# Performance work log

Hardware: AMD Instinct MI355X
Metric: run time of the kernel (lower is better)

The kernel has to match this reference:

```python
import jax, jax.numpy as jnp
import numpy as np

B, T, IN, HID, OUT, NB = 64, 150, 120, 1024, 35, 8
VTH = 1.0


def _branch_mask(rng, out_dim, in_size):
    # For each output neuron: a random permutation of inputs split into NB equal branches.
    perm = np.argsort(rng.random((out_dim, in_size)), axis=1)          # [out, in]
    branch = (np.arange(in_size) * NB) // in_size                      # branch id of each slot
    rows = (np.arange(out_dim)[:, None] * NB + branch[None, :]).ravel()
    m = np.zeros((out_dim * NB, in_size), dtype=np.bool_)
    m[rows, perm.ravel()] = True
    return jnp.asarray(m)


def setup_inputs() -> dict:
    rng = np.random.default_rng(0)

    def lin(o, i):
        bound = 1.0 / np.sqrt(i)
        w = rng.uniform(-bound, bound, (o, i)).astype(np.float32)
        b = rng.uniform(-bound, bound, (o,)).astype(np.float32)
        return jnp.asarray(w), jnp.asarray(b)

    def tau(*shape):
        return jnp.asarray(rng.uniform(0.0, 4.0, shape).astype(np.float32))

    w1, b1 = lin(HID * NB, IN)
    w2, b2 = lin(HID * NB, HID)
    w3, b3 = lin(HID * NB, HID)
    wr, br = lin(OUT, HID)

    x = jax.random.normal(jax.random.key(0), (B, 1, T, IN), dtype=jnp.float32)

    return dict(
        x=x,
        w1=w1, b1=b1, tau_m1=tau(HID), tau_n1=tau(HID, NB),
        w2=w2, b2=b2, tau_m2=tau(HID), tau_n2=tau(HID, NB),
        w3=w3, b3=b3, tau_m3=tau(HID), tau_n3=tau(HID, NB),
        wr=wr, br=br, tau_mr=tau(OUT),
        mask1=_branch_mask(rng, HID, IN),
        mask2=_branch_mask(rng, HID, HID),
        mask3=_branch_mask(rng, HID, HID),
    )


@jax.custom_vjp
def act_fun(x):  # spike with rectangular surrogate gradient
    return (x > 0.0).astype(x.dtype)

def _act_fwd(x):
    return act_fun(x), x

def _act_bwd(x, g):
    return (g * (jnp.abs(x) < 0.5).astype(g.dtype),)

act_fun.defvjp(_act_fwd, _act_bwd)


def _dh_step(spk_in, d, mem, spk, wm, b, tau_m, tau_n):
    # wm: pre-masked weight [HID*NB, D_in]
    dense = (spk_in @ wm.T + b).reshape(-1, HID, NB)      # [B, HID, NB]
    beta = jax.nn.sigmoid(tau_n)                          # [HID, NB]
    d = beta * d + (1.0 - beta) * dense                   # branch decay
    l_input = d.sum(axis=2)                               # [B, HID]
    alpha = jax.nn.sigmoid(tau_m)
    mem = mem * alpha + (1.0 - alpha) * l_input - VTH * spk  # soft reset (prev spike)
    spk = act_fun(mem - VTH)
    return d, mem, spk


def _forward(x, w1, b1, tau_m1, tau_n1, w2, b2, tau_m2, tau_n2,
             w3, b3, tau_m3, tau_n3, wr, br, tau_mr, mask1, mask2, mask3):
    b_sz = x.shape[0]
    wm1 = w1 * mask1.astype(w1.dtype)
    wm2 = w2 * mask2.astype(w2.dtype)
    wm3 = w3 * mask3.astype(w3.dtype)
    alpha_r = jax.nn.sigmoid(tau_mr)

    xt = x[:, 0].transpose(1, 0, 2)                        # [T, B, IN]

    z_bh = jnp.zeros((b_sz, HID), x.dtype)
    z_bhn = jnp.zeros((b_sz, HID, NB), x.dtype)
    carry0 = (z_bhn, z_bh, z_bh, z_bhn, z_bh, z_bh, z_bhn, z_bh, z_bh,
              jnp.zeros((b_sz, OUT), x.dtype), jnp.zeros((b_sz, OUT), x.dtype))

    def step(carry, inp_t):
        d1, m1, s1, d2, m2, s2, d3, m3, s3, mr, acc = carry
        d1, m1, s1 = _dh_step(inp_t, d1, m1, s1, wm1, b1, tau_m1, tau_n1)
        d2, m2, s2 = _dh_step(s1,    d2, m2, s2, wm2, b2, tau_m2, tau_n2)
        d3, m3, s3 = _dh_step(s2,    d3, m3, s3, wm3, b3, tau_m3, tau_n3)
        mr = mr * alpha_r + (1.0 - alpha_r) * (s3 @ wr.T + br)
        acc = acc + mr
        return (d1, m1, s1, d2, m2, s2, d3, m3, s3, mr, acc), None

    (_, _, _, _, _, _, _, _, _, _, acc), _ = jax.lax.scan(step, carry0, xt)
    return jax.nn.log_softmax(acc / xt.shape[0], axis=1)


def reference(x, w1, b1, tau_m1, tau_n1, w2, b2, tau_m2, tau_n2,
              w3, b3, tau_m3, tau_n3, wr, br, tau_mr, mask1, mask2, mask3):
    return _forward(x, w1, b1, tau_m1, tau_n1, w2, b2, tau_m2, tau_n2,
                    w3, b3, tau_m3, tau_n3, wr, br, tau_mr, mask1, mask2, mask3)
```

## Files before the change

### kernel.cpp

```cpp
#include <hip/hip_runtime.h>
#include <stdint.h>

#define BATCH 64
#define TT    150
#define INSZ  120
#define HID   1024
#define OUTN  35
#define NBR   8
#define TPAD  160
#define CH    8
#define NCHUNK 19

typedef __attribute__((address_space(4))) const uint64_t cu64;

#define XT_OFF  0
#define S1_OFF  4608000
#define S2_OFF  5918720
#define S3_OFF  7229440
#define Y_OFF   8540160
#define ACC_OFF 9884160

__global__ __launch_bounds__(256) void k_tx(const float* __restrict__ x,
                                            float* __restrict__ xT) {
    const int t = blockIdx.x;
    __shared__ float tile[INSZ * 65];
    for (int e = threadIdx.x; e < INSZ * 64; e += 256) {
        const int b = e / INSZ, i = e - b * INSZ;
        tile[i * 65 + b] = x[((size_t)b * TT + t) * INSZ + i];
    }
    __syncthreads();
    for (int e = threadIdx.x; e < INSZ * 64; e += 256) {
        const int i = e >> 6, b = e & 63;
        xT[((size_t)t * INSZ + i) * 64 + b] = tile[i * 65 + b];
    }
}

template <int DIN, int NNZ, int MODE>
__global__ __launch_bounds__(512, 8) void k_layer(
    const float* __restrict__ w,
    const void* __restrict__ maskp,
    const float* __restrict__ bias,
    const float* __restrict__ tau_m,
    const float* __restrict__ tau_n,
    const float* __restrict__ xin,
    const uint64_t* __restrict__ inm,
    uint64_t* __restrict__ outm)
{
    const int tid  = threadIdx.x;
    const int lane = tid & 63;
    const int wid  = tid >> 6;
    const int h    = blockIdx.x;
    const int r    = h * NBR + wid;

    __shared__ uint2 ent[NBR * NNZ];
    __shared__ float red[2][NBR * CH * 64];

    inm = (const uint64_t*)__builtin_assume_aligned(inm, 64);

    const unsigned char* m8  = (const unsigned char*)maskp;
    const int*           m32 = (const int*)maskp;
    {
        const int base = wid * NNZ;
        int cnt = 0;
        for (int c = 0; c * 64 < DIN; ++c) {
            const int i = c * 64 + lane;
            int   mv = 0;
            float wv = 0.f;
            if (i < DIN) {
                mv = m8[(size_t)r * DIN + i];
                wv = w[(size_t)r * DIN + i];
            }
            const unsigned long long bal = __ballot(mv != 0);
            const int pos = __popcll(bal & ((1ull << lane) - 1ull));
            if (mv && cnt + pos < NNZ)
                ent[base + cnt + pos] = make_uint2(__float_as_uint(wv), (unsigned)i);
            cnt += __popcll(bal);
        }
        if (cnt != NNZ) {
            cnt = 0;
            for (int c = 0; c * 64 < DIN; ++c) {
                const int i = c * 64 + lane;
                int   mv = 0;
                float wv = 0.f;
                if (i < DIN) {
                    mv = m32[(size_t)r * DIN + i];
                    wv = w[(size_t)r * DIN + i];
                }
                const unsigned long long bal = __ballot(mv != 0);
                const int pos = __popcll(bal & ((1ull << lane) - 1ull));
                if (mv) ent[base + cnt + pos] =
                            make_uint2(__float_as_uint(wv), (unsigned)i);
                cnt += __popcll(bal);
            }
        }
    }
    __syncthreads();

    const float be = 1.f / (1.f + expf(-tau_n[r]));
    const float om = 1.f - be;
    const float bb = bias[r];
    const float al  = 1.f / (1.f + expf(-tau_m[h]));
    const float oma = 1.f - al;

    float d = 0.f, mem = 0.f, spkprev = 0.f;
    const int base = wid * NNZ;

    for (int tc = 0; tc < NCHUNK; ++tc) {
        const int t0  = tc * CH;
        const int buf = tc & 1;
        float a[CH];
#pragma unroll
        for (int k = 0; k < CH; ++k) a[k] = 0.f;

        if constexpr (MODE == 1) {
#pragma unroll 4
            for (int j = 0; j < NNZ; ++j) {
                const uint2 e  = ent[base + j];
                const int   ix = __builtin_amdgcn_readfirstlane((int)e.y);
                const float wv = __uint_as_float(e.x);
                const cu64* p = (const cu64*)(inm + (size_t)ix * TPAD + t0);
                uint64_t m[CH];
#pragma unroll
                for (int k = 0; k < CH; ++k) m[k] = p[k];
#pragma unroll
                for (int k = 0; k < CH; ++k) {
                    float s;
                    asm("v_cndmask_b32 %0, 0, %1, %2"
                        : "=v"(s) : "v"(wv), "s"(m[k]));
                    a[k] += s;
                }
            }
        } else {
            const float* xb = xin + (size_t)t0 * DIN * 64;
#pragma unroll 3
            for (int j = 0; j < NNZ; ++j) {
                const uint2 e  = ent[base + j];
                const int   ix = __builtin_amdgcn_readfirstlane((int)e.y);
                const float wv = __uint_as_float(e.x);
#pragma unroll
                for (int k = 0; k < CH; ++k)
                    a[k] += wv * xb[((size_t)k * DIN + ix) * 64 + lane];
            }
        }

#pragma unroll
        for (int k = 0; k < CH; ++k) {
            d = be * d + om * (a[k] + bb);
            red[buf][(wid * CH + k) * 64 + lane] = d;
        }
        __syncthreads();

        if (wid == 0) {
#pragma unroll
            for (int k = 0; k < CH; ++k) {
                const float r0 = red[buf][(0 * CH + k) * 64 + lane];
                const float r1 = red[buf][(1 * CH + k) * 64 + lane];
                const float r2 = red[buf][(2 * CH + k) * 64 + lane];
                const float r3 = red[buf][(3 * CH + k) * 64 + lane];
                const float r4 = red[buf][(4 * CH + k) * 64 + lane];
                const float r5 = red[buf][(5 * CH + k) * 64 + lane];
                const float r6 = red[buf][(6 * CH + k) * 64 + lane];
                const float r7 = red[buf][(7 * CH + k) * 64 + lane];
                const float p01 = r0 + r1, p23 = r2 + r3;
                const float p45 = r4 + r5, p67 = r6 + r7;
                const float l = ((p01 + p23) + p45) + p67;
                if (t0 + k < TT) {
                    mem = al * mem + oma * l - spkprev;
                    spkprev = (mem > 1.0f) ? 1.f : 0.f;
                    const unsigned long long bal = __ballot(mem > 1.0f);
                    if (lane == 0) outm[(size_t)h * TPAD + (t0 + k)] = bal;
                }
            }
        }
    }
}

__global__ __launch_bounds__(256) void k_ry(const float* __restrict__ wr,
                                            const uint64_t* __restrict__ s3m,
                                            float* __restrict__ Y) {
    const int lane  = threadIdx.x & 63;
    const int wid   = __builtin_amdgcn_readfirstlane(threadIdx.x >> 6);
    const int o  = blockIdx.x / NCHUNK;
    const int t0 = (blockIdx.x % NCHUNK) * CH;
    s3m = (const uint64_t*)__builtin_assume_aligned(s3m, 64);
    const float* wrow = wr + (size_t)o * HID;
    __shared__ float red[4 * CH * 64];
    float acc[CH];
#pragma unroll
    for (int k = 0; k < CH; ++k) acc[k] = 0.f;
#pragma unroll 4
    for (int ii = 0; ii < HID / 4; ++ii) {
        const int i = wid * (HID / 4) + ii;
        const float wv = wrow[i];
        const cu64* p = (const cu64*)(s3m + (size_t)i * TPAD + t0);
        uint64_t m[CH];
#pragma unroll
        for (int k = 0; k < CH; ++k) m[k] = p[k];
#pragma unroll
        for (int k = 0; k < CH; ++k) {
            float s;
            asm("v_cndmask_b32 %0, 0, %1, %2" : "=v"(s) : "v"(wv), "s"(m[k]));
            acc[k] += s;
        }
    }
#pragma unroll
    for (int k = 0; k < CH; ++k)
        red[(wid * CH + k) * 64 + lane] = acc[k];
    __syncthreads();
    if (wid == 0) {
#pragma unroll
        for (int k = 0; k < CH; ++k) {
            if (t0 + k >= TT) break;
            const float v = ((red[(0 * CH + k) * 64 + lane]
                            + red[(1 * CH + k) * 64 + lane])
                            + red[(2 * CH + k) * 64 + lane])
                            + red[(3 * CH + k) * 64 + lane];
            Y[((size_t)(t0 + k) * OUTN + o) * 64 + lane] = v;
        }
    }
}

__global__ void k_racc(const float* __restrict__ Y,
                       const float* __restrict__ br,
                       const float* __restrict__ tau_mr,
                       float* __restrict__ ACC) {
    const int o = blockIdx.x, lane = threadIdx.x;
    const float ar  = 1.f / (1.f + expf(-tau_mr[o]));
    const float bro = br[o];
    float acc = 0.f, q = ar;
    for (int t = TT - 1; t >= 0; --t) {
        const float y = Y[((size_t)t * OUTN + o) * 64 + lane] + bro;
        acc += y * (1.f - q);
        q *= ar;
    }
    ACC[o * 64 + lane] = acc;
}

__global__ void k_smax(const float* __restrict__ ACC, float* __restrict__ out) {
    const int b = threadIdx.x;
    float v[OUTN];
    float mx = -3.4e38f;
    for (int o = 0; o < OUTN; ++o) {
        v[o] = ACC[o * 64 + b] / (float)TT;
        mx = fmaxf(mx, v[o]);
    }
    float sum = 0.f;
    for (int o = 0; o < OUTN; ++o) sum += expf(v[o] - mx);
    const float lse = mx + logf(sum);
    for (int o = 0; o < OUTN; ++o) out[b * OUTN + o] = v[o] - lse;
}

extern "C" void kernel_launch(void* const* d_in, const int* in_sizes, int n_in,
                              void* d_out, int out_size, void* d_ws,
                              size_t ws_size, hipStream_t stream) {
    (void)in_sizes; (void)n_in; (void)out_size; (void)ws_size;
    const float* x   = (const float*)d_in[0];
    const float* w1  = (const float*)d_in[1];
    const float* b1  = (const float*)d_in[2];
    const float* tm1 = (const float*)d_in[3];
    const float* tn1 = (const float*)d_in[4];
    const float* w2  = (const float*)d_in[5];
    const float* b2  = (const float*)d_in[6];
    const float* tm2 = (const float*)d_in[7];
    const float* tn2 = (const float*)d_in[8];
    const float* w3  = (const float*)d_in[9];
    const float* b3  = (const float*)d_in[10];
    const float* tm3 = (const float*)d_in[11];
    const float* tn3 = (const float*)d_in[12];
    const float* wr  = (const float*)d_in[13];
    const float* br  = (const float*)d_in[14];
    const float* tmr = (const float*)d_in[15];
    const void*  m1  = d_in[16];
    const void*  m2  = d_in[17];
    const void*  m3  = d_in[18];
    float* out = (float*)d_out;

    char* ws = (char*)d_ws;
    float*    xT  = (float*)(ws + XT_OFF);
    uint64_t* s1m = (uint64_t*)(ws + S1_OFF);
    uint64_t* s2m = (uint64_t*)(ws + S2_OFF);
    uint64_t* s3m = (uint64_t*)(ws + S3_OFF);
    float*    Y   = (float*)(ws + Y_OFF);
    float*    ACC = (float*)(ws + ACC_OFF);

    k_tx<<<TT, 256, 0, stream>>>(x, xT);
    k_layer<INSZ, 15, 0><<<HID, 512, 0, stream>>>(
        w1, m1, b1, tm1, tn1, xT, nullptr, s1m);
    k_layer<HID, 128, 1><<<HID, 512, 0, stream>>>(
        w2, m2, b2, tm2, tn2, nullptr, s1m, s2m);
    k_layer<HID, 128, 1><<<HID, 512, 0, stream>>>(
        w3, m3, b3, tm3, tn3, nullptr, s2m, s3m);
    k_ry<<<OUTN * NCHUNK, 256, 0, stream>>>(wr, s3m, Y);
    k_racc<<<OUTN, 64, 0, stream>>>(Y, br, tmr, ACC);
    k_smax<<<1, 64, 0, stream>>>(ACC, out);
}
```

Before: 1.622 ms.

## Precompact sparse weights to global memory and use wide scalar loads

Moves the per-row mask compaction for layers 2 and 3 out of the layer kernel into a separate k_cmp kernel that writes compacted weight and index arrays to the workspace. The layer kernel then reads those arrays with 8-wide scalar vector loads instead of going through LDS, and fetches the 8 spike bitmasks per input as one 512-bit scalar load. The readout kernel uses the same wide load. The aim is to cut LDS traffic and the readfirstlane step in the inner loop and to issue fewer, wider scalar memory operations. In exchange it adds two kernel launches and an extra global round trip through the workspace.

```diff
diff --git a/kernel.cpp b/kernel.cpp
--- a/kernel.cpp
+++ b/kernel.cpp
@@ -10,8 +10,14 @@
 #define TPAD  160
 #define CH    8
 #define NCHUNK 19
-
-typedef __attribute__((address_space(4))) const uint64_t cu64;
+#define NNZC  128
+
+typedef unsigned long long u64x8 __attribute__((ext_vector_type(8)));
+typedef int   i32x8 __attribute__((ext_vector_type(8)));
+typedef float f32x8 __attribute__((ext_vector_type(8)));
+typedef __attribute__((address_space(4))) const u64x8 cu64x8;
+typedef __attribute__((address_space(4))) const i32x8 ci32x8;
+typedef __attribute__((address_space(4))) const f32x8 cf32x8;
 
 #define XT_OFF  0
 #define S1_OFF  4608000
@@ -19,6 +25,10 @@
 #define S3_OFF  7229440
 #define Y_OFF   8540160
 #define ACC_OFF 9884160
+#define WC2_OFF 9893120
+#define IC2_OFF 14087424
+#define WC3_OFF 18281728
+#define IC3_OFF 22476032
 
 __global__ __launch_bounds__(256) void k_tx(const float* __restrict__ x,
                                             float* __restrict__ xT) {
@@ -32,6 +42,41 @@
     for (int e = threadIdx.x; e < INSZ * 64; e += 256) {
         const int i = e >> 6, b = e & 63;
         xT[((size_t)t * INSZ + i) * 64 + b] = tile[i * 65 + b];
+    }
+}
+
+__global__ __launch_bounds__(512) void k_cmp(const float* __restrict__ w,
+                                             const void* __restrict__ maskp,
+                                             float* __restrict__ wcomp,
+                                             int* __restrict__ icomp) {
+    const int lane = threadIdx.x & 63;
+    const int wid  = threadIdx.x >> 6;
+    const int r    = blockIdx.x * NBR + wid;
+    const unsigned char* m8  = (const unsigned char*)maskp;
+    const int*           m32 = (const int*)maskp;
+    float* wout = wcomp + (size_t)r * NNZC;
+    int*   iout = icomp + (size_t)r * NNZC;
+    int cnt = 0;
+    for (int c = 0; c * 64 < HID; ++c) {
+        const int i = c * 64 + lane;
+        const int   mv = m8[(size_t)r * HID + i];
+        const float wv = w[(size_t)r * HID + i];
+        const unsigned long long bal = __ballot(mv != 0);
+        const int pos = __popcll(bal & ((1ull << lane) - 1ull));
+        if (mv && cnt + pos < NNZC) { wout[cnt + pos] = wv; iout[cnt + pos] = i; }
+        cnt += __popcll(bal);
+    }
+    if (cnt != NNZC) {
+        cnt = 0;
+        for (int c = 0; c * 64 < HID; ++c) {
+            const int i = c * 64 + lane;
+            const int   mv = m32[(size_t)r * HID + i];
+            const float wv = w[(size_t)r * HID + i];
+            const unsigned long long bal = __ballot(mv != 0);
+            const int pos = __popcll(bal & ((1ull << lane) - 1ull));
+            if (mv) { wout[cnt + pos] = wv; iout[cnt + pos] = i; }
+            cnt += __popcll(bal);
+        }
     }
 }
 
@@ -44,22 +89,24 @@
     const float* __restrict__ tau_n,
     const float* __restrict__ xin,
     const uint64_t* __restrict__ inm,
+    const float* __restrict__ wcomp,
+    const int* __restrict__ icomp,
     uint64_t* __restrict__ outm)
 {
     const int tid  = threadIdx.x;
     const int lane = tid & 63;
-    const int wid  = tid >> 6;
+    const int wid  = __builtin_amdgcn_readfirstlane(tid >> 6);
     const int h    = blockIdx.x;
     const int r    = h * NBR + wid;
 
-    __shared__ uint2 ent[NBR * NNZ];
+    __shared__ uint2 ent[(MODE == 0) ? (NBR * NNZ) : 1];
     __shared__ float red[2][NBR * CH * 64];
 
     inm = (const uint64_t*)__builtin_assume_aligned(inm, 64);
 
-    const unsigned char* m8  = (const unsigned char*)maskp;
-    const int*           m32 = (const int*)maskp;
-    {
+    if constexpr (MODE == 0) {
+        const unsigned char* m8  = (const unsigned char*)maskp;
+        const int*           m32 = (const int*)maskp;
         const int base = wid * NNZ;
         int cnt = 0;
         for (int c = 0; c * 64 < DIN; ++c) {
@@ -93,8 +140,8 @@
                 cnt += __popcll(bal);
             }
         }
-    }
-    __syncthreads();
+        __syncthreads();
+    }
 
     const float be = 1.f / (1.f + expf(-tau_n[r]));
     const float om = 1.f - be;
@@ -103,7 +150,6 @@
     const float oma = 1.f - al;
 
     float d = 0.f, mem = 0.f, spkprev = 0.f;
-    const int base = wid * NNZ;
 
     for (int tc = 0; tc < NCHUNK; ++tc) {
         const int t0  = tc * CH;
@@ -113,24 +159,29 @@
         for (int k = 0; k < CH; ++k) a[k] = 0.f;
 
         if constexpr (MODE == 1) {
-#pragma unroll 4
-            for (int j = 0; j < NNZ; ++j) {
-                const uint2 e  = ent[base + j];
-                const int   ix = __builtin_amdgcn_readfirstlane((int)e.y);
-                const float wv = __uint_as_float(e.x);
-                const cu64* p = (const cu64*)(inm + (size_t)ix * TPAD + t0);
-                uint64_t m[CH];
-#pragma unroll
-                for (int k = 0; k < CH; ++k) m[k] = p[k];
-#pragma unroll
-                for (int k = 0; k < CH; ++k) {
-                    float s;
-                    asm("v_cndmask_b32 %0, 0, %1, %2"
-                        : "=v"(s) : "v"(wv), "s"(m[k]));
-                    a[k] += s;
+            const float* __restrict__ wcp = wcomp + (size_t)r * NNZ;
+            const int*   __restrict__ icp = icomp + (size_t)r * NNZ;
+            static_assert(NNZ % 8 == 0, "NNZ multiple of 8");
+#pragma unroll 2
+            for (int jb = 0; jb < NNZ / 8; ++jb) {
+                const i32x8 ix8 = *(const ci32x8*)(icp + jb * 8);
+                const f32x8 wv8 = *(const cf32x8*)(wcp + jb * 8);
+#pragma unroll
+                for (int jj = 0; jj < 8; ++jj) {
+                    const u64x8 m =
+                        *(const cu64x8*)(inm + (size_t)ix8[jj] * TPAD + t0);
+                    const float wv = wv8[jj];
+#pragma unroll
+                    for (int k = 0; k < CH; ++k) {
+                        float s;
+                        asm("v_cndmask_b32 %0, 0, %1, %2"
+                            : "=v"(s) : "v"(wv), "s"(m[k]));
+                        a[k] += s;
+                    }
                 }
             }
         } else {
+            const int base = wid * NNZ;
             const float* xb = xin + (size_t)t0 * DIN * 64;
 #pragma unroll 3
             for (int j = 0; j < NNZ; ++j) {
@@ -192,10 +243,7 @@
     for (int ii = 0; ii < HID / 4; ++ii) {
         const int i = wid * (HID / 4) + ii;
         const float wv = wrow[i];
-        const cu64* p = (const cu64*)(s3m + (size_t)i * TPAD + t0);
-        uint64_t m[CH];
-#pragma unroll
-        for (int k = 0; k < CH; ++k) m[k] = p[k];
+        const u64x8 m = *(const cu64x8*)(s3m + (size_t)i * TPAD + t0);
 #pragma unroll
         for (int k = 0; k < CH; ++k) {
             float s;
@@ -282,14 +330,20 @@
     uint64_t* s3m = (uint64_t*)(ws + S3_OFF);
     float*    Y   = (float*)(ws + Y_OFF);
     float*    ACC = (float*)(ws + ACC_OFF);
+    float*    wc2 = (float*)(ws + WC2_OFF);
+    int*      ic2 = (int*)(ws + IC2_OFF);
+    float*    wc3 = (float*)(ws + WC3_OFF);
+    int*      ic3 = (int*)(ws + IC3_OFF);
 
     k_tx<<<TT, 256, 0, stream>>>(x, xT);
+    k_cmp<<<HID, 512, 0, stream>>>(w2, m2, wc2, ic2);
+    k_cmp<<<HID, 512, 0, stream>>>(w3, m3, wc3, ic3);
     k_layer<INSZ, 15, 0><<<HID, 512, 0, stream>>>(
-        w1, m1, b1, tm1, tn1, xT, nullptr, s1m);
-    k_layer<HID, 128, 1><<<HID, 512, 0, stream>>>(
-        w2, m2, b2, tm2, tn2, nullptr, s1m, s2m);
-    k_layer<HID, 128, 1><<<HID, 512, 0, stream>>>(
-        w3, m3, b3, tm3, tn3, nullptr, s2m, s3m);
+        w1, m1, b1, tm1, tn1, xT, nullptr, nullptr, nullptr, s1m);
+    k_layer<HID, NNZC, 1><<<HID, 512, 0, stream>>>(
+        w2, m2, b2, tm2, tn2, nullptr, s1m, wc2, ic2, s2m);
+    k_layer<HID, NNZC, 1><<<HID, 512, 0, stream>>>(
+        w3, m3, b3, tm3, tn3, nullptr, s2m, wc3, ic3, s3m);
     k_ry<<<OUTN * NCHUNK, 256, 0, stream>>>(wr, s3m, Y);
     k_racc<<<OUTN, 64, 0, stream>>>(Y, br, tmr, ACC);
     k_smax<<<1, 64, 0, stream>>>(ACC, out);
```

After: 1.712 ms. 5.6% more time.
